# Kernel tuning notes

Measured on AMD Instinct MI355X. Metric: run time of the kernel, lower is better.

## Reference

```python
import jax, jax.numpy as jnp
import numpy as np
import math

B = 65536
N_NUM = 64; N_CAT = 16; CAT_SIZE = 1000; EMB = 16
ND = 64; NA = 64; OUT = ND + NA; NSTEPS = 5; GAMMA = 1.5
NFEAT = N_NUM + N_CAT * EMB          # 320
NGROUPS = N_NUM + N_CAT              # 80
GROUP_IDX = np.repeat(np.arange(NGROUPS), [1] * N_NUM + [EMB] * N_CAT)  # len 320
RES_SCALE = math.sqrt(0.5)
BN_EPS = 1e-5


def setup_inputs() -> dict:
    keys = iter(jax.random.split(jax.random.key(0), 64))
    def rn(shape, std):
        return jax.random.normal(next(keys), shape, jnp.float32) * std
    def mk_bn(c, lead=()):
        # stacked (scale, bias, running_mean, running_var) along axis -2
        s = 1.0 + 0.05 * jax.random.normal(next(keys), (*lead, c), jnp.float32)
        b = 0.05 * jax.random.normal(next(keys), (*lead, c), jnp.float32)
        m = 0.05 * jax.random.normal(next(keys), (*lead, c), jnp.float32)
        v = 1.0 + 0.1 * jax.random.uniform(next(keys), (*lead, c), dtype=jnp.float32)
        return jnp.stack([s, b, m, v], axis=-2)
    inp = {}
    inp["x_num"] = jax.random.normal(next(keys), (B, N_NUM), jnp.float32)
    inp["x_cat"] = jax.random.randint(next(keys), (B, N_CAT), 0, CAT_SIZE)
    inp["emb_W"] = rn((N_CAT, CAT_SIZE, EMB), 0.1)
    inp["in_bn"] = mk_bn(NFEAT)
    inp["sh_W0"] = rn((NFEAT, 2 * OUT), 1.0 / math.sqrt(NFEAT))
    inp["sh_b0"] = jnp.zeros((2 * OUT,), jnp.float32)
    inp["sh_bn0"] = mk_bn(2 * OUT)
    inp["sh_W1"] = rn((OUT, 2 * OUT), 1.0 / math.sqrt(OUT))
    inp["sh_b1"] = jnp.zeros((2 * OUT,), jnp.float32)
    inp["sh_bn1"] = mk_bn(2 * OUT)
    inp["init_W"] = rn((2, OUT, 2 * OUT), 1.0 / math.sqrt(OUT))
    inp["init_b"] = jnp.zeros((2, 2 * OUT), jnp.float32)
    inp["init_bn"] = mk_bn(2 * OUT, (2,))
    inp["step_W"] = rn((NSTEPS, 2, OUT, 2 * OUT), 1.0 / math.sqrt(OUT))
    inp["step_b"] = jnp.zeros((NSTEPS, 2, 2 * OUT), jnp.float32)
    inp["step_bn"] = mk_bn(2 * OUT, (NSTEPS, 2))
    inp["att_W"] = rn((NSTEPS, NA, NGROUPS), 1.0 / math.sqrt(NA))
    inp["att_b"] = jnp.zeros((NSTEPS, NGROUPS), jnp.float32)
    inp["att_bn"] = mk_bn(NGROUPS, (NSTEPS,))
    inp["out_W"] = rn((ND, 1), 1.0 / math.sqrt(ND))
    inp["out_b"] = jnp.zeros((1,), jnp.float32)
    return inp


def bn_apply(x, p):
    s, b, m, v = p  # each [C]
    return (x - m) * jax.lax.rsqrt(v + BN_EPS) * s + b


def glu_layer(x, W, b, bn):
    h = bn_apply(x @ W + b, bn)          # [B, 2*OUT]
    o, g = jnp.split(h, 2, axis=1)
    return o * jax.nn.sigmoid(g)


def glu_block(x, W, b, bn):
    y = glu_layer(x, W, b, bn)
    return (x + y) * RES_SCALE if x.shape == y.shape else y


def sparsemax(z):
    # along axis=1; Martins & Astudillo 2016
    zs = -jnp.sort(-z, axis=1)
    cs = jnp.cumsum(zs, axis=1)
    r = jnp.arange(1, z.shape[1] + 1, dtype=z.dtype)
    support = (1.0 + r * zs) > cs
    k = jnp.maximum(support.sum(axis=1, keepdims=True), 1)
    cs_k = jnp.take_along_axis(cs, k - 1, axis=1)
    tau = (cs_k - 1.0) / k.astype(z.dtype)
    return jnp.maximum(z - tau, 0.0)


def _forward(x_num, x_cat, emb_W, in_bn, sh_W0, sh_b0, sh_bn0, sh_W1, sh_b1, sh_bn1,
             init_W, init_b, init_bn, step_W, step_b, step_bn, att_W, att_b, att_bn,
             out_W, out_b):
    # categorical embeddings: [B, N_CAT, EMB] -> [B, N_CAT*EMB]
    emb = emb_W[np.arange(N_CAT)[None, :], x_cat].reshape(x_cat.shape[0], -1)
    x = jnp.concatenate([x_num, emb], axis=1)  # [B, NFEAT]
    x = bn_apply(x, in_bn)

    def ft_shared(h):
        h = glu_block(h, sh_W0, sh_b0, sh_bn0)   # 320 -> 128, no residual
        return glu_block(h, sh_W1, sh_b1, sh_bn1)  # residual

    def ft_indep(h, W, b, bn):
        for i in range(W.shape[0]):
            h = glu_block(h, W[i], b[i], bn[i])
        return h

    out0 = ft_indep(ft_shared(x), init_W, init_b, init_bn)
    a = out0[:, ND:]
    prior = jnp.ones((x.shape[0], NGROUPS), x.dtype)
    decision_sum = jnp.zeros((x.shape[0], ND), x.dtype)
    for step in range(NSTEPS):
        logits = bn_apply(a @ att_W[step] + att_b[step], att_bn[step]) * prior
        mask_group = sparsemax(logits)           # [B, NGROUPS]
        prior = prior * (GAMMA - mask_group)
        mask = mask_group[:, GROUP_IDX]          # [B, NFEAT] (repeat_interleave)
        out = ft_indep(ft_shared(mask * x), step_W[step], step_b[step], step_bn[step])
        d, a = out[:, :ND], out[:, ND:]
        decision_sum = decision_sum + jax.nn.relu(d)
    return decision_sum @ out_W + out_b          # [B, 1]


def reference(x_num, x_cat, emb_W, in_bn, sh_W0, sh_b0, sh_bn0, sh_W1, sh_b1, sh_bn1,
              init_W, init_b, init_bn, step_W, step_b, step_bn, att_W, att_b, att_bn,
              out_W, out_b):
    return _forward(x_num, x_cat, emb_W, in_bn, sh_W0, sh_b0, sh_bn0, sh_W1, sh_b1,
                    sh_bn1, init_W, init_b, init_bn, step_W, step_b, step_bn,
                    att_W, att_b, att_bn, out_W, out_b)
```

## Files before the change

kernel.cpp:

```cpp
#include <hip/hip_runtime.h>
#include <math.h>
#include <stdint.h>

typedef _Float16 half_t;
typedef _Float16 half8 __attribute__((ext_vector_type(8)));
typedef __fp16 fp16x2 __attribute__((ext_vector_type(2)));
typedef float floatx4 __attribute__((ext_vector_type(4)));
typedef float floatx16 __attribute__((ext_vector_type(16)));

constexpr float BN_EPS_C = 1e-5f;
constexpr float RES_SCALE_C = 0.70710678118654752f;
constexpr float GAMMA_C = 1.5f;
#define B_TOT 65536

__device__ __forceinline__ uint32_t pack2(float y) {
    const half_t h = (half_t)y;
    const half_t l = (half_t)(y - (float)h);
    union { half_t f; unsigned short u; } a, b; a.f = h; b.f = l;
    return (uint32_t)a.u | ((uint32_t)b.u << 16);
}
__device__ __forceinline__ void unpack2(uint32_t v, half_t& h, half_t& l) {
    union { unsigned short u; half_t f; } a, b;
    a.u = (unsigned short)(v & 0xffffu); b.u = (unsigned short)(v >> 16);
    h = a.f; l = b.f;
}
__device__ __forceinline__ void split_pair(float y0, float y1, half_t& h0, half_t& l0, half_t& h1, half_t& l1) {
    fp16x2 hh = __builtin_amdgcn_cvt_pkrtz(y0, y1);
    fp16x2 ll = __builtin_amdgcn_cvt_pkrtz(y0 - (float)hh.x, y1 - (float)hh.y);
    h0 = (half_t)hh.x; l0 = (half_t)ll.x; h1 = (half_t)hh.y; l1 = (half_t)ll.y;
}
__device__ __forceinline__ void pack2_pair(float y0, float y1, uint32_t& w0, uint32_t& w1) {
    fp16x2 hh = __builtin_amdgcn_cvt_pkrtz(y0, y1);
    fp16x2 ll = __builtin_amdgcn_cvt_pkrtz(y0 - (float)hh.x, y1 - (float)hh.y);
    const uint32_t hb = __builtin_bit_cast(uint32_t, hh);
    const uint32_t lb = __builtin_bit_cast(uint32_t, ll);
    w0 = (hb & 0xffffu) | (lb << 16);
    w1 = (hb >> 16) | (lb & 0xffff0000u);
}

__global__ void wsplit_kernel(const float* __restrict__ sh_W0, const float* __restrict__ sh_W1,
                              const float* __restrict__ init_W, const float* __restrict__ step_W,
                              half_t* __restrict__ Wh, half_t* __restrict__ Wl)
{
    const int b = blockIdx.x, n = threadIdx.x;
    const float* src; int k; size_t base;
    if (b < 320)      { src = sh_W0;           k = b;       base = 0; }
    else if (b < 448) { src = sh_W1;           k = b - 320; base = 81920; }
    else if (b < 576) { src = init_W;          k = b - 448; base = 114688; }
    else if (b < 704) { src = init_W + 32768;  k = b - 576; base = 147456; }
    else {
        int j = (b - 704) >> 7; k = (b - 704) & 127;
        src = step_W + (size_t)j * 32768; base = 180224 + (size_t)j * 32768;
    }
    const float v = src[k * 256 + n];
    const half_t hi = (half_t)v;
    const half_t lo = (half_t)(v - (float)hi);
    const size_t idx = base + (size_t)(((k >> 3) * 256 + n) * 8 + (k & 7));
    Wh[idx] = hi; Wl[idx] = lo;
}

__global__ void wsplit_att_kernel(const float* __restrict__ att_W,
                                  half_t* __restrict__ aWh, half_t* __restrict__ aWl)
{
    const int b = blockIdx.x;
    const int n = threadIdx.x;
    const int step = b >> 6, k = b & 63;
    const float v = att_W[(size_t)b * 80 + n];
    const half_t h = (half_t)v;
    const half_t l = (half_t)(v - (float)h);
    const size_t idx = (size_t)step * 5120 + (size_t)(((k >> 3) * 80 + n) * 8 + (k & 7));
    aWh[idx] = h; aWl[idx] = l;
}

__global__ void embed_bn_kernel(const float* __restrict__ x_num, const int* __restrict__ x_cat,
                                const float* __restrict__ emb_W, const float* __restrict__ in_bn,
                                uint32_t* __restrict__ xp)
{
    const int idx = blockIdx.x * 256 + threadIdx.x;
    const int s = idx / 320, j = idx - s * 320;
    float v;
    if (j < 64) v = x_num[(size_t)s * 64 + j];
    else {
        const int c = (j - 64) >> 4, e = (j - 64) & 15;
        v = emb_W[(size_t)(c * 1000 + x_cat[(size_t)s * 16 + c]) * 16 + e];
    }
    const float val = (v - in_bn[640 + j]) * (in_bn[j] * __frsqrt_rn(in_bn[960 + j] + BN_EPS_C)) + in_bn[320 + j];
    xp[idx] = pack2(val);
}

__device__ __forceinline__ void bn_fold(const float* __restrict__ bn, const float* __restrict__ bias,
                                        int c, float& sc, float& sh)
{
    sc = bn[c] * __frsqrt_rn(bn[768 + c] + BN_EPS_C);
    sh = fmaf(bias[c] - bn[512 + c], sc, bn[256 + c]);
}

__device__ __forceinline__ float glu_val(float accO, float accG,
                                         float sc_o, float sh_o, float sc_g, float sh_g)
{
    const float o = fmaf(accO, sc_o, sh_o);
    const float g = fmaf(accG, sc_g, sh_g);
    const float e = __expf(-g);
    return o * __builtin_amdgcn_rcpf(1.f + e);
}

#define MFMA32(A, B, C) C = __builtin_amdgcn_mfma_f32_32x32x16_f16(A, B, C, 0, 0, 0)
#define MFMA16(A, B, C) C = __builtin_amdgcn_mfma_f32_16x16x32_f16(A, B, C, 0, 0, 0)

__device__ __forceinline__ void layer_accum(const half_t (*H_h)[136], const half_t (*H_l)[136],
                                            const half_t* __restrict__ Wh, const half_t* __restrict__ Wl,
                                            size_t off, int n32, int k8, int no, int m0, int rot,
                                            floatx16* accO, floatx16* accG)
{
#pragma unroll 2
    for (int s = 0; s < 8; ++s) {
        const int sl8 = (s + rot) & 7;
        const int kq = sl8 * 2 + k8;
        const size_t wo = off + (size_t)(kq * 256 + no + n32) * 8;
        const half8 bo_h = *(const half8*)(Wh + wo);
        const half8 bo_l = *(const half8*)(Wl + wo);
        const half8 bg_h = *(const half8*)(Wh + wo + 1024);
        const half8 bg_l = *(const half8*)(Wl + wo + 1024);
#pragma unroll
        for (int mt = 0; mt < 2; ++mt) {
            const half8 a_h = *(const half8*)&H_h[m0 + mt * 32 + n32][sl8 * 16 + k8 * 8];
            const half8 a_l = *(const half8*)&H_l[m0 + mt * 32 + n32][sl8 * 16 + k8 * 8];
            MFMA32(a_h, bo_h, accO[mt]); MFMA32(a_h, bg_h, accG[mt]);
            MFMA32(a_l, bo_h, accO[mt]); MFMA32(a_l, bg_h, accG[mt]);
            MFMA32(a_h, bo_l, accO[mt]); MFMA32(a_h, bg_l, accG[mt]);
        }
    }
}

template<bool MASK>
__global__ __launch_bounds__(512, 4)
void ft_chain(const uint32_t* __restrict__ xp, uint32_t* __restrict__ avp,
              const half_t* __restrict__ Wh, const half_t* __restrict__ Wl,
              const half_t* __restrict__ aWh, const half_t* __restrict__ aWl,
              const float* __restrict__ att_b, const float* __restrict__ att_bn,
              float* __restrict__ prior,
              const float* __restrict__ b1, const float* __restrict__ bn1,
              const float* __restrict__ b2, const float* __restrict__ bn2,
              const float* __restrict__ b3, const float* __restrict__ bn3,
              const float* __restrict__ b4, const float* __restrict__ bn4,
              size_t w3_off, size_t w4_off,
              float* __restrict__ ds, int wmode_last, int step)
{
    __shared__ __align__(16) char smem[79872];
    float    (*mgs)[84]  = (float    (*)[84])smem;
    half_t   (*As_h)[72] = (half_t   (*)[72])(smem + 43008);
    half_t   (*As_l)[72] = (half_t   (*)[72])(smem + 61440);
    uint32_t (*Apk)[68]  = (uint32_t (*)[68])(smem + 43008);
    half_t   (*H_h)[136] = (half_t   (*)[136])smem;
    half_t   (*H_l)[136] = (half_t   (*)[136])(smem + 34816);

    const int t = threadIdx.x;
    const int s0 = blockIdx.x * 128;
    const int w = t >> 6, lane = t & 63;
    const int wq = w & 3, wh = w >> 2;
    const int n32 = lane & 31, k8 = lane >> 5;
    const int quad = lane >> 4, l16 = lane & 15;
    const int no = 32 * wq;
    const int m0 = wh * 64;
    const int half_id = (blockIdx.x >> 8) & 1;
    const int rowA = t >> 2, kA = (t & 3) * 16;

    if (MASK) {
        {
            const uint4* src = (const uint4*)(avp + (size_t)(s0 + rowA) * 64 + kA);
            uint4* dst = (uint4*)&Apk[rowA][kA];
#pragma unroll
            for (int q = 0; q < 4; ++q) dst[q] = src[q];
        }
        __syncthreads();
        floatx4 zacc[5];
#pragma unroll
        for (int nt = 0; nt < 5; ++nt) zacc[nt] = (floatx4){0.f, 0.f, 0.f, 0.f};
#pragma unroll
        for (int kc = 0; kc < 64; kc += 32) {
            uint32_t wv[8];
            *(uint4*)&wv[0] = *(const uint4*)&Apk[w * 16 + l16][kc + quad * 8];
            *(uint4*)&wv[4] = *(const uint4*)&Apk[w * 16 + l16][kc + quad * 8 + 4];
            half8 a_h, a_l;
#pragma unroll
            for (int j = 0; j < 8; ++j) { half_t h, l; unpack2(wv[j], h, l); a_h[j] = h; a_l[j] = l; }
            const int kq = (kc >> 3) + quad;
#pragma unroll
            for (int nt = 0; nt < 5; ++nt) {
                const size_t wi = (size_t)(kq * 80 + nt * 16 + l16) * 8;
                const half8 b_h = *(const half8*)(aWh + wi);
                const half8 b_l = *(const half8*)(aWl + wi);
                MFMA16(a_h, b_h, zacc[nt]);
                MFMA16(a_l, b_h, zacc[nt]);
                MFMA16(a_h, b_l, zacc[nt]);
            }
        }
        float preg[5][4];
#pragma unroll
        for (int nt = 0; nt < 5; ++nt) {
            const int c = nt * 16 + l16;
            const float sc = att_bn[c] * __frsqrt_rn(att_bn[240 + c] + BN_EPS_C);
            const float sh = fmaf(att_b[c] - att_bn[160 + c], sc, att_bn[80 + c]);
#pragma unroll
            for (int r = 0; r < 4; ++r) {
                const int sl = w * 16 + quad * 4 + r;
                const float pr = (step == 0) ? 1.f : prior[(size_t)(s0 + sl) * 80 + c];
                preg[nt][r] = pr;
                mgs[sl][c] = fmaf(zacc[nt][r], sc, sh) * pr;
            }
        }
        __syncthreads();
        {
            const int samp = rowA, j0 = (t & 3) * 20;
            float zj[20], zmax = -1e30f;
#pragma unroll
            for (int j = 0; j < 20; ++j) { zj[j] = mgs[samp][j0 + j]; zmax = fmaxf(zmax, zj[j]); }
            zmax = fmaxf(zmax, __shfl_xor(zmax, 1));
            zmax = fmaxf(zmax, __shfl_xor(zmax, 2));
            float lo = zmax - 1.f, hi = zmax;
#pragma unroll 1
            for (int it = 0; it < 16; ++it) {
                const float mid = 0.5f * (lo + hi);
                float ssum = 0.f;
#pragma unroll
                for (int j = 0; j < 20; ++j) ssum += fmaxf(zj[j] - mid, 0.f);
                ssum += __shfl_xor(ssum, 1);
                ssum += __shfl_xor(ssum, 2);
                if (ssum >= 1.f) lo = mid; else hi = mid;
            }
            const float tau = 0.5f * (lo + hi);
#pragma unroll
            for (int j = 0; j < 20; ++j) mgs[samp][j0 + j] = fmaxf(zj[j] - tau, 0.f);
        }
        __syncthreads();
#pragma unroll
        for (int nt = 0; nt < 5; ++nt) {
            const int c = nt * 16 + l16;
#pragma unroll
            for (int r = 0; r < 4; ++r) {
                const int sl = w * 16 + quad * 4 + r;
                prior[(size_t)(s0 + sl) * 80 + c] = preg[nt][r] * (GAMMA_C - mgs[sl][c]);
            }
        }
    }

    floatx16 accO[2], accG[2];
#pragma unroll
    for (int i = 0; i < 2; ++i) { accO[i] = (floatx16)(0.f); accG[i] = (floatx16)(0.f); }

    const uint32_t* arow = xp + (size_t)(s0 + rowA) * 320 + kA;
    uint32_t pfw[16];
    int ic = half_id * 2;
#pragma unroll
    for (int q = 0; q < 4; ++q)
        *(uint4*)&pfw[q * 4] = *(const uint4*)(arow + ic * 64 + q * 4);

#pragma unroll 1
    for (int i = 0; i < 5; ++i) {
        __syncthreads();
        {
            const int kb = ic * 64 + kA;
            float mG = 1.f;
            if (MASK && ic != 0) mG = mgs[rowA][64 + ((kb - 64) >> 4)];
#pragma unroll
            for (int q = 0; q < 2; ++q) {
                half8 hh, ll;
                if (MASK && ic == 0) {
#pragma unroll
                    for (int j = 0; j < 8; ++j) {
                        half_t h, l; unpack2(pfw[q * 8 + j], h, l);
                        const float v = ((float)h + (float)l) * mgs[rowA][kb + q * 8 + j];
                        const half_t nh = (half_t)v;
                        hh[j] = nh; ll[j] = (half_t)(v - (float)nh);
                    }
                } else if (MASK) {
#pragma unroll
                    for (int j = 0; j < 8; ++j) {
                        half_t h, l; unpack2(pfw[q * 8 + j], h, l);
                        const float v = ((float)h + (float)l) * mG;
                        const half_t nh = (half_t)v;
                        hh[j] = nh; ll[j] = (half_t)(v - (float)nh);
                    }
                } else {
#pragma unroll
                    for (int j = 0; j < 8; ++j) { half_t h, l; unpack2(pfw[q * 8 + j], h, l); hh[j] = h; ll[j] = l; }
                }
                *(half8*)&As_h[rowA][kA + q * 8] = hh;
                *(half8*)&As_l[rowA][kA + q * 8] = ll;
            }
        }
        __syncthreads();
        const int icn = (ic + 1 == 5) ? 0 : ic + 1;
        if (i < 4) {
#pragma unroll
            for (int q = 0; q < 4; ++q)
                *(uint4*)&pfw[q * 4] = *(const uint4*)(arow + icn * 64 + q * 4);
        }
#pragma unroll
        for (int sl4 = 0; sl4 < 4; ++sl4) {
            const int kq = ic * 8 + sl4 * 2 + k8;
            const size_t wo = (size_t)(kq * 256 + no + n32) * 8;
            const half8 bo_h = *(const half8*)(Wh + wo);
            const half8 bo_l = *(const half8*)(Wl + wo);
            const half8 bg_h = *(const half8*)(Wh + wo + 1024);
            const half8 bg_l = *(const half8*)(Wl + wo + 1024);
#pragma unroll
            for (int mt = 0; mt < 2; ++mt) {
                const half8 a_h = *(const half8*)&As_h[m0 + mt * 32 + n32][sl4 * 16 + k8 * 8];
                const half8 a_l = *(const half8*)&As_l[m0 + mt * 32 + n32][sl4 * 16 + k8 * 8];
                MFMA32(a_h, bo_h, accO[mt]); MFMA32(a_h, bg_h, accG[mt]);
                MFMA32(a_l, bo_h, accO[mt]); MFMA32(a_l, bg_h, accG[mt]);
                MFMA32(a_h, bo_l, accO[mt]); MFMA32(a_h, bg_l, accG[mt]);
            }
        }
        ic = icn;
    }
    __syncthreads();

    {
        const int c = no + n32;
        float sc_o, sh_o, sc_g, sh_g;
        bn_fold(bn1, b1, c, sc_o, sh_o);
        bn_fold(bn1, b1, c + 128, sc_g, sh_g);
#pragma unroll
        for (int mt = 0; mt < 2; ++mt)
#pragma unroll
            for (int q = 0; q < 4; ++q)
#pragma unroll
                for (int rp = 0; rp < 2; ++rp) {
                    const int r0 = q * 4 + rp * 2;
                    const int sl = m0 + mt * 32 + rp * 2 + 8 * q + 4 * k8;
                    const float y0 = glu_val(accO[mt][r0],     accG[mt][r0],     sc_o, sh_o, sc_g, sh_g);
                    const float y1 = glu_val(accO[mt][r0 + 1], accG[mt][r0 + 1], sc_o, sh_o, sc_g, sh_g);
                    half_t h0, l0, h1, l1;
                    split_pair(y0, y1, h0, l0, h1, l1);
                    H_h[sl][c] = h0; H_l[sl][c] = l0;
                    H_h[sl + 1][c] = h1; H_l[sl + 1][c] = l1;
                }
    }
    __syncthreads();

#pragma unroll 1
    for (int layer = 0; layer < 2; ++layer) {
        const float* bb = layer ? b3 : b2;
        const float* bn = layer ? bn3 : bn2;
        const size_t off = layer ? w3_off : (size_t)81920;
#pragma unroll
        for (int i = 0; i < 2; ++i) { accO[i] = (floatx16)(0.f); accG[i] = (floatx16)(0.f); }
        layer_accum(H_h, H_l, Wh, Wl, off, n32, k8, no, m0, half_id * 4, accO, accG);
        __syncthreads();
        {
            const int c = no + n32;
            float sc_o, sh_o, sc_g, sh_g;
            bn_fold(bn, bb, c, sc_o, sh_o);
            bn_fold(bn, bb, c + 128, sc_g, sh_g);
#pragma unroll
            for (int mt = 0; mt < 2; ++mt)
#pragma unroll
                for (int q = 0; q < 4; ++q)
#pragma unroll
                    for (int rp = 0; rp < 2; ++rp) {
                        const int r0 = q * 4 + rp * 2;
                        const int sl = m0 + mt * 32 + rp * 2 + 8 * q + 4 * k8;
                        const float res0 = (float)H_h[sl][c] + (float)H_l[sl][c];
                        const float res1 = (float)H_h[sl + 1][c] + (float)H_l[sl + 1][c];
                        const float y0 = (glu_val(accO[mt][r0],     accG[mt][r0],     sc_o, sh_o, sc_g, sh_g) + res0) * RES_SCALE_C;
                        const float y1 = (glu_val(accO[mt][r0 + 1], accG[mt][r0 + 1], sc_o, sh_o, sc_g, sh_g) + res1) * RES_SCALE_C;
                        half_t h0, l0, h1, l1;
                        split_pair(y0, y1, h0, l0, h1, l1);
                        H_h[sl][c] = h0; H_l[sl][c] = l0;
                        H_h[sl + 1][c] = h1; H_l[sl + 1][c] = l1;
                    }
        }
        __syncthreads();
    }

#pragma unroll
    for (int i = 0; i < 2; ++i) { accO[i] = (floatx16)(0.f); accG[i] = (floatx16)(0.f); }
    layer_accum(H_h, H_l, Wh, Wl, w4_off, n32, k8, no, m0, half_id * 4, accO, accG);
    {
        const int c = no + n32;
        float sc_o, sh_o, sc_g, sh_g;
        bn_fold(bn4, b4, c, sc_o, sh_o);
        bn_fold(bn4, b4, c + 128, sc_g, sh_g);
        if (wq < 2) {
            if (wmode_last != 1) {
#pragma unroll
                for (int mt = 0; mt < 2; ++mt)
#pragma unroll
                    for (int reg = 0; reg < 16; ++reg) {
                        const int sl = m0 + mt * 32 + (reg & 3) + 8 * (reg >> 2) + 4 * k8;
                        const float res = (float)H_h[sl][c] + (float)H_l[sl][c];
                        const float y = (glu_val(accO[mt][reg], accG[mt][reg], sc_o, sh_o, sc_g, sh_g) + res) * RES_SCALE_C;
                        const float d = fmaxf(y, 0.f);
                        float* dp = ds + (size_t)(s0 + sl) * 64 + c;
                        *dp = (wmode_last == 2) ? d : (*dp + d);
                    }
            }
        } else {
#pragma unroll
            for (int mt = 0; mt < 2; ++mt)
#pragma unroll
                for (int q = 0; q < 4; ++q)
#pragma unroll
                    for (int rp = 0; rp < 2; ++rp) {
                        const int r0 = q * 4 + rp * 2;
                        const int sl = m0 + mt * 32 + rp * 2 + 8 * q + 4 * k8;
                        const float res0 = (float)H_h[sl][c] + (float)H_l[sl][c];
                        const float res1 = (float)H_h[sl + 1][c] + (float)H_l[sl + 1][c];
                        const float y0 = (glu_val(accO[mt][r0],     accG[mt][r0],     sc_o, sh_o, sc_g, sh_g) + res0) * RES_SCALE_C;
                        const float y1 = (glu_val(accO[mt][r0 + 1], accG[mt][r0 + 1], sc_o, sh_o, sc_g, sh_g) + res1) * RES_SCALE_C;
                        uint32_t w0, w1;
                        pack2_pair(y0, y1, w0, w1);
                        avp[(size_t)(s0 + sl) * 64 + (c - 64)] = w0;
                        avp[(size_t)(s0 + sl + 1) * 64 + (c - 64)] = w1;
                    }
        }
    }
}

__global__ void final_kernel(const float* __restrict__ dsum, const float* __restrict__ out_W,
                             const float* __restrict__ out_b, float* __restrict__ out)
{
    const int s = blockIdx.x * 256 + threadIdx.x;
    float acc = out_b[0];
    const float4* dp = (const float4*)(dsum + (size_t)s * 64);
    const float4* wp = (const float4*)out_W;
#pragma unroll
    for (int q = 0; q < 16; ++q) {
        const float4 d = dp[q];
        const float4 ww = wp[q];
        acc += d.x * ww.x + d.y * ww.y + d.z * ww.z + d.w * ww.w;
    }
    out[s] = acc;
}

extern "C" void kernel_launch(void* const* d_in, const int* in_sizes, int n_in,
                              void* d_out, int out_size, void* d_ws, size_t ws_size,
                              hipStream_t stream)
{
    const float* x_num  = (const float*)d_in[0];
    const int*   x_cat  = (const int*)d_in[1];
    const float* emb_W  = (const float*)d_in[2];
    const float* in_bn  = (const float*)d_in[3];
    const float* sh_W0  = (const float*)d_in[4];
    const float* sh_b0  = (const float*)d_in[5];
    const float* sh_bn0 = (const float*)d_in[6];
    const float* sh_W1  = (const float*)d_in[7];
    const float* sh_b1  = (const float*)d_in[8];
    const float* sh_bn1 = (const float*)d_in[9];
    const float* init_W = (const float*)d_in[10];
    const float* init_b = (const float*)d_in[11];
    const float* init_bn= (const float*)d_in[12];
    const float* step_W = (const float*)d_in[13];
    const float* step_b = (const float*)d_in[14];
    const float* step_bn= (const float*)d_in[15];
    const float* att_W  = (const float*)d_in[16];
    const float* att_b  = (const float*)d_in[17];
    const float* att_bn = (const float*)d_in[18];
    const float* out_W  = (const float*)d_in[19];
    const float* out_b  = (const float*)d_in[20];

    const size_t B = B_TOT;
    char* p = (char*)d_ws;
    uint32_t* xp  = (uint32_t*)p;  p += B * 320 * 4;
    uint32_t* avp = (uint32_t*)p;  p += B * 64 * 4;
    half_t* Wh    = (half_t*)p;    p += 507904 * 2;
    half_t* Wl    = (half_t*)p;    p += 507904 * 2;
    half_t* aWh   = (half_t*)p;    p += 25600 * 2;
    half_t* aWl   = (half_t*)p;    p += 25600 * 2;
    float* pri    = (float*)p;     p += B * 80 * 4;
    float* ds     = (float*)p;     p += B * 64 * 4;

    wsplit_kernel<<<1984, 256, 0, stream>>>(sh_W0, sh_W1, init_W, step_W, Wh, Wl);
    wsplit_att_kernel<<<320, 80, 0, stream>>>(att_W, aWh, aWl);
    embed_bn_kernel<<<(B_TOT * 320) / 256, 256, 0, stream>>>(x_num, x_cat, emb_W, in_bn, xp);

    const int GB = B_TOT / 128;
    ft_chain<false><<<GB, 512, 0, stream>>>(xp, avp, Wh, Wl,
                                            nullptr, nullptr, nullptr, nullptr, nullptr,
                                            sh_b0, sh_bn0, sh_b1, sh_bn1,
                                            init_b, init_bn, init_b + 256, init_bn + 1024,
                                            (size_t)114688, (size_t)147456, ds, 1, 0);
    for (int st = 0; st < 5; ++st) {
        const size_t w3 = 180224 + (size_t)(st * 2 + 0) * 32768;
        const size_t w4 = 180224 + (size_t)(st * 2 + 1) * 32768;
        ft_chain<true><<<GB, 512, 0, stream>>>(xp, avp, Wh, Wl,
                                               aWh + st * 5120, aWl + st * 5120,
                                               att_b + st * 80, att_bn + st * 320, pri,
                                               sh_b0, sh_bn0, sh_b1, sh_bn1,
                                               step_b + (st * 2 + 0) * 256, step_bn + (st * 2 + 0) * 1024,
                                               step_b + (st * 2 + 1) * 256, step_bn + (st * 2 + 1) * 1024,
                                               w3, w4, ds, st == 0 ? 2 : 3, st);
    }
    final_kernel<<<B_TOT / 256, 256, 0, stream>>>(ds, out_W, out_b, (float*)d_out);
}
```

Baseline: 733.3 us.

## Double-buffer first-layer A tiles and fold residual scale into weights

```diff
diff --git a/kernel.cpp b/kernel.cpp
--- a/kernel.cpp
+++ b/kernel.cpp
@@ -36,6 +36,13 @@
     const uint32_t lb = __builtin_bit_cast(uint32_t, ll);
     w0 = (hb & 0xffffu) | (lb << 16);
     w1 = (hb >> 16) | (lb & 0xffff0000u);
+}
+__device__ __forceinline__ void unpack8(const uint32_t* wv, half8& h, half8& l) {
+#pragma unroll
+    for (int j = 0; j < 8; ++j) {
+        half_t hh, ll; unpack2(wv[j], hh, ll);
+        h[j] = hh; l[j] = ll;
+    }
 }
 
 __global__ void wsplit_kernel(const float* __restrict__ sh_W0, const float* __restrict__ sh_W1,
@@ -52,7 +59,8 @@
         int j = (b - 704) >> 7; k = (b - 704) & 127;
         src = step_W + (size_t)j * 32768; base = 180224 + (size_t)j * 32768;
     }
-    const float v = src[k * 256 + n];
+    float v = src[k * 256 + n];
+    if (b >= 448) v *= RES_SCALE_C;
     const half_t hi = (half_t)v;
     const half_t lo = (half_t)(v - (float)hi);
     const size_t idx = base + (size_t)(((k >> 3) * 256 + n) * 8 + (k & 7));
@@ -65,7 +73,7 @@
     const int b = blockIdx.x;
     const int n = threadIdx.x;
     const int step = b >> 6, k = b & 63;
-    const float v = att_W[(size_t)b * 80 + n];
+    const float v = att_W[(size_t)b * 80 + n] * RES_SCALE_C;
     const half_t h = (half_t)v;
     const half_t l = (half_t)(v - (float)h);
     const size_t idx = (size_t)step * 5120 + (size_t)(((k >> 3) * 80 + n) * 8 + (k & 7));
@@ -148,9 +156,9 @@
 {
     __shared__ __align__(16) char smem[79872];
     float    (*mgs)[84]  = (float    (*)[84])smem;
-    half_t   (*As_h)[72] = (half_t   (*)[72])(smem + 43008);
-    half_t   (*As_l)[72] = (half_t   (*)[72])(smem + 61440);
     uint32_t (*Apk)[68]  = (uint32_t (*)[68])(smem + 43008);
+    uint32_t (*As0)[36]  = (uint32_t (*)[36])(smem + 43008);
+    uint32_t (*As1)[36]  = (uint32_t (*)[36])(smem + 61440);
     half_t   (*H_h)[136] = (half_t   (*)[136])smem;
     half_t   (*H_l)[136] = (half_t   (*)[136])(smem + 34816);
 
@@ -163,12 +171,13 @@
     const int no = 32 * wq;
     const int m0 = wh * 64;
     const int half_id = (blockIdx.x >> 8) & 1;
-    const int rowA = t >> 2, kA = (t & 3) * 16;
+    const int rowA = t >> 2, kA8 = (t & 3) * 8;
 
     if (MASK) {
         {
-            const uint4* src = (const uint4*)(avp + (size_t)(s0 + rowA) * 64 + kA);
-            uint4* dst = (uint4*)&Apk[rowA][kA];
+            const int kA16 = (t & 3) * 16;
+            const uint4* src = (const uint4*)(avp + (size_t)(s0 + rowA) * 64 + kA16);
+            uint4* dst = (uint4*)&Apk[rowA][kA16];
 #pragma unroll
             for (int q = 0; q < 4; ++q) dst[q] = src[q];
         }
@@ -182,8 +191,7 @@
             *(uint4*)&wv[0] = *(const uint4*)&Apk[w * 16 + l16][kc + quad * 8];
             *(uint4*)&wv[4] = *(const uint4*)&Apk[w * 16 + l16][kc + quad * 8 + 4];
             half8 a_h, a_l;
-#pragma unroll
-            for (int j = 0; j < 8; ++j) { half_t h, l; unpack2(wv[j], h, l); a_h[j] = h; a_l[j] = l; }
+            unpack8(wv, a_h, a_l);
             const int kq = (kc >> 3) + quad;
 #pragma unroll
             for (int nt = 0; nt < 5; ++nt) {
@@ -248,57 +256,64 @@
 #pragma unroll
     for (int i = 0; i < 2; ++i) { accO[i] = (floatx16)(0.f); accG[i] = (floatx16)(0.f); }
 
-    const uint32_t* arow = xp + (size_t)(s0 + rowA) * 320 + kA;
-    uint32_t pfw[16];
-    int ic = half_id * 2;
-#pragma unroll
-    for (int q = 0; q < 4; ++q)
-        *(uint4*)&pfw[q * 4] = *(const uint4*)(arow + ic * 64 + q * 4);
+    const uint32_t* arow = xp + (size_t)(s0 + rowA) * 320 + kA8;
+    uint32_t pfw[2][8];
+    const int ic0 = half_id * 5;
+
+    auto stage_half = [&](uint32_t (*Asb)[36], int c, int sl2, const uint32_t* pf) {
+        const int kb = c * 32 + kA8 + sl2 * 4;
+        uint4 out;
+        if (MASK) {
+            float m[4];
+            if (c < 2) {
+                const float4 mq = *(const float4*)&mgs[rowA][kb];
+                m[0] = mq.x; m[1] = mq.y; m[2] = mq.z; m[3] = mq.w;
+            } else {
+                const float mg = mgs[rowA][64 + ((kb - 64) >> 4)];
+                m[0] = m[1] = m[2] = m[3] = mg;
+            }
+            float y[4];
+#pragma unroll
+            for (int j = 0; j < 4; ++j) {
+                half_t h, l; unpack2(pf[sl2 * 4 + j], h, l);
+                y[j] = ((float)h + (float)l) * m[j];
+            }
+            uint32_t w0, w1, w2, w3;
+            pack2_pair(y[0], y[1], w0, w1);
+            pack2_pair(y[2], y[3], w2, w3);
+            out = make_uint4(w0, w1, w2, w3);
+        } else {
+            out = *(const uint4*)&pf[sl2 * 4];
+        }
+        *(uint4*)&Asb[rowA][kA8 + sl2 * 4] = out;
+    };
+
+    {
+        *(uint4*)&pfw[0][0] = *(const uint4*)(arow + ic0 * 32);
+        *(uint4*)&pfw[0][4] = *(const uint4*)(arow + ic0 * 32 + 4);
+        stage_half(As0, ic0, 0, pfw[0]);
+        stage_half(As0, ic0, 1, pfw[0]);
+        const int c1 = (ic0 + 1) % 10;
+        *(uint4*)&pfw[1][0] = *(const uint4*)(arow + c1 * 32);
+        *(uint4*)&pfw[1][4] = *(const uint4*)(arow + c1 * 32 + 4);
+    }
+    __syncthreads();
 
 #pragma unroll 1
-    for (int i = 0; i < 5; ++i) {
-        __syncthreads();
-        {
-            const int kb = ic * 64 + kA;
-            float mG = 1.f;
-            if (MASK && ic != 0) mG = mgs[rowA][64 + ((kb - 64) >> 4)];
-#pragma unroll
-            for (int q = 0; q < 2; ++q) {
-                half8 hh, ll;
-                if (MASK && ic == 0) {
-#pragma unroll
-                    for (int j = 0; j < 8; ++j) {
-                        half_t h, l; unpack2(pfw[q * 8 + j], h, l);
-                        const float v = ((float)h + (float)l) * mgs[rowA][kb + q * 8 + j];
-                        const half_t nh = (half_t)v;
-                        hh[j] = nh; ll[j] = (half_t)(v - (float)nh);
-                    }
-                } else if (MASK) {
-#pragma unroll
-                    for (int j = 0; j < 8; ++j) {
-                        half_t h, l; unpack2(pfw[q * 8 + j], h, l);
-                        const float v = ((float)h + (float)l) * mG;
-                        const half_t nh = (half_t)v;
-                        hh[j] = nh; ll[j] = (half_t)(v - (float)nh);
-                    }
-                } else {
-#pragma unroll
-                    for (int j = 0; j < 8; ++j) { half_t h, l; unpack2(pfw[q * 8 + j], h, l); hh[j] = h; ll[j] = l; }
-                }
-                *(half8*)&As_h[rowA][kA + q * 8] = hh;
-                *(half8*)&As_l[rowA][kA + q * 8] = ll;
-            }
-        }
-        __syncthreads();
-        const int icn = (ic + 1 == 5) ? 0 : ic + 1;
-        if (i < 4) {
-#pragma unroll
-            for (int q = 0; q < 4; ++q)
-                *(uint4*)&pfw[q * 4] = *(const uint4*)(arow + icn * 64 + q * 4);
-        }
-#pragma unroll
-        for (int sl4 = 0; sl4 < 4; ++sl4) {
-            const int kq = ic * 8 + sl4 * 2 + k8;
+    for (int i = 0; i < 10; ++i) {
+        const int cc = (ic0 + i) % 10;
+        const int cn = (cc + 1 == 10) ? 0 : cc + 1;
+        uint32_t (*AsC)[36] = (i & 1) ? As1 : As0;
+        uint32_t (*AsN)[36] = (i & 1) ? As0 : As1;
+        if (i <= 7) {
+            const int c2 = (ic0 + i + 2) % 10;
+            *(uint4*)&pfw[i & 1][0] = *(const uint4*)(arow + c2 * 32);
+            *(uint4*)&pfw[i & 1][4] = *(const uint4*)(arow + c2 * 32 + 4);
+        }
+#pragma unroll
+        for (int sl4 = 0; sl4 < 2; ++sl4) {
+            if (i < 9) stage_half(AsN, cn, sl4, pfw[(i + 1) & 1]);
+            const int kq = cc * 4 + sl4 * 2 + k8;
             const size_t wo = (size_t)(kq * 256 + no + n32) * 8;
             const half8 bo_h = *(const half8*)(Wh + wo);
             const half8 bo_l = *(const half8*)(Wl + wo);
@@ -306,16 +321,18 @@
             const half8 bg_l = *(const half8*)(Wl + wo + 1024);
 #pragma unroll
             for (int mt = 0; mt < 2; ++mt) {
-                const half8 a_h = *(const half8*)&As_h[m0 + mt * 32 + n32][sl4 * 16 + k8 * 8];
-                const half8 a_l = *(const half8*)&As_l[m0 + mt * 32 + n32][sl4 * 16 + k8 * 8];
+                uint32_t wv[8];
+                *(uint4*)&wv[0] = *(const uint4*)&AsC[m0 + mt * 32 + n32][sl4 * 16 + k8 * 8];
+                *(uint4*)&wv[4] = *(const uint4*)&AsC[m0 + mt * 32 + n32][sl4 * 16 + k8 * 8 + 4];
+                half8 a_h, a_l;
+                unpack8(wv, a_h, a_l);
                 MFMA32(a_h, bo_h, accO[mt]); MFMA32(a_h, bg_h, accG[mt]);
                 MFMA32(a_l, bo_h, accO[mt]); MFMA32(a_l, bg_h, accG[mt]);
                 MFMA32(a_h, bo_l, accO[mt]); MFMA32(a_h, bg_l, accG[mt]);
             }
         }
-        ic = icn;
-    }
-    __syncthreads();
+        __syncthreads();
+    }
 
     {
         const int c = no + n32;
@@ -345,6 +362,7 @@
         const float* bb = layer ? b3 : b2;
         const float* bn = layer ? bn3 : bn2;
         const size_t off = layer ? w3_off : (size_t)81920;
+        const float rs = layer ? RES_SCALE_C : 1.0f;
 #pragma unroll
         for (int i = 0; i < 2; ++i) { accO[i] = (floatx16)(0.f); accG[i] = (floatx16)(0.f); }
         layer_accum(H_h, H_l, Wh, Wl, off, n32, k8, no, m0, half_id * 4, accO, accG);
@@ -364,8 +382,8 @@
                         const int sl = m0 + mt * 32 + rp * 2 + 8 * q + 4 * k8;
                         const float res0 = (float)H_h[sl][c] + (float)H_l[sl][c];
                         const float res1 = (float)H_h[sl + 1][c] + (float)H_l[sl + 1][c];
-                        const float y0 = (glu_val(accO[mt][r0],     accG[mt][r0],     sc_o, sh_o, sc_g, sh_g) + res0) * RES_SCALE_C;
-                        const float y1 = (glu_val(accO[mt][r0 + 1], accG[mt][r0 + 1], sc_o, sh_o, sc_g, sh_g) + res1) * RES_SCALE_C;
+                        const float y0 = fmaf(rs, res0, glu_val(accO[mt][r0],     accG[mt][r0],     sc_o, sh_o, sc_g, sh_g));
+                        const float y1 = fmaf(rs, res1, glu_val(accO[mt][r0 + 1], accG[mt][r0 + 1], sc_o, sh_o, sc_g, sh_g));
                         half_t h0, l0, h1, l1;
                         split_pair(y0, y1, h0, l0, h1, l1);
                         H_h[sl][c] = h0; H_l[sl][c] = l0;
@@ -391,7 +409,7 @@
                     for (int reg = 0; reg < 16; ++reg) {
                         const int sl = m0 + mt * 32 + (reg & 3) + 8 * (reg >> 2) + 4 * k8;
                         const float res = (float)H_h[sl][c] + (float)H_l[sl][c];
-                        const float y = (glu_val(accO[mt][reg], accG[mt][reg], sc_o, sh_o, sc_g, sh_g) + res) * RES_SCALE_C;
+                        const float y = fmaf(RES_SCALE_C, res, glu_val(accO[mt][reg], accG[mt][reg], sc_o, sh_o, sc_g, sh_g));
                         const float d = fmaxf(y, 0.f);
                         float* dp = ds + (size_t)(s0 + sl) * 64 + c;
                         *dp = (wmode_last == 2) ? d : (*dp + d);
@@ -408,8 +426,8 @@
                         const int sl = m0 + mt * 32 + rp * 2 + 8 * q + 4 * k8;
                         const float res0 = (float)H_h[sl][c] + (float)H_l[sl][c];
                         const float res1 = (float)H_h[sl + 1][c] + (float)H_l[sl + 1][c];
-                        const float y0 = (glu_val(accO[mt][r0],     accG[mt][r0],     sc_o, sh_o, sc_g, sh_g) + res0) * RES_SCALE_C;
-                        const float y1 = (glu_val(accO[mt][r0 + 1], accG[mt][r0 + 1], sc_o, sh_o, sc_g, sh_g) + res1) * RES_SCALE_C;
+                        const float y0 = fmaf(RES_SCALE_C, res0, glu_val(accO[mt][r0],     accG[mt][r0],     sc_o, sh_o, sc_g, sh_g));
+                        const float y1 = fmaf(RES_SCALE_C, res1, glu_val(accO[mt][r0 + 1], accG[mt][r0 + 1], sc_o, sh_o, sc_g, sh_g));
                         uint32_t w0, w1;
                         pack2_pair(y0, y1, w0, w1);
                         avp[(size_t)(s0 + sl) * 64 + (c - 64)] = w0;
@@ -423,7 +441,7 @@
                              const float* __restrict__ out_b, float* __restrict__ out)
 {
     const int s = blockIdx.x * 256 + threadIdx.x;
-    float acc = out_b[0];
+    float acc = 0.f;
     const float4* dp = (const float4*)(dsum + (size_t)s * 64);
     const float4* wp = (const float4*)out_W;
 #pragma unroll
@@ -432,7 +450,7 @@
         const float4 ww = wp[q];
         acc += d.x * ww.x + d.y * ww.y + d.z * ww.z + d.w * ww.w;
     }
-    out[s] = acc;
+    out[s] = fmaf(RES_SCALE_C, acc, out_b[0]);
 }
 
 extern "C" void kernel_launch(void* const* d_in, const int* in_sizes, int n_in,
```

Result: slower. 780.2 us (+6.4%).
